# Optimization experiments

Measured on AMD Instinct MI355X. Metric: run time of the kernel, lower is better.

Reference implementation:

```python
import jax, jax.numpy as jnp
import numpy as np
from jax import lax

Q = 12           # sliding window size
IN_LEN = 336     # input_length
OUT_LEN = 336    # output_length


def setup_inputs() -> dict:
    key = jax.random.key(0)
    history_data = jax.random.normal(key, (64, IN_LEN, 862, 3), dtype=jnp.float32)
    return {"history_data": history_data}


def reference(history_data):
    # Maintain a rolling window of the last Q frames instead of torch.cat growth.
    window = history_data[:, -Q:, :, :]  # [B, Q, N, C]

    def step(w, _):
        m = jnp.mean(w, axis=1)  # [B, N, C]
        w = jnp.concatenate([w[:, 1:], m[:, None]], axis=1)  # shift window
        return w, m

    _, means = lax.scan(step, window, None, length=OUT_LEN)  # [O, B, N, C]
    prediction = jnp.transpose(means, (1, 0, 2, 3))  # [B, O, N, C]
    return prediction
```

## Files before the change

kernel.cpp:

```cpp
#include <hip/hip_runtime.h>


#define Q 12
#define IN_LEN 336
#define OUT_LEN 336
#define NB 64
#define SC (862 * 3)

__global__ __launch_bounds__(256) void
SimpleMovingAverage_22144851378808_kernel(const float* __restrict__ in,
                                          float* __restrict__ out) {
    const int tid = blockIdx.x * blockDim.x + threadIdx.x;
    if (tid >= NB * SC) return;
    const int b  = tid / SC;
    const int sc = tid - b * SC;

    const float* inp = in + ((size_t)(b * IN_LEN + (IN_LEN - Q)) * SC + sc);
    float w[Q];
#pragma unroll
    for (int k = 0; k < Q; ++k) w[k] = inp[(size_t)k * SC];

    float sum = 0.f;
#pragma unroll
    for (int k = 0; k < Q; ++k) sum += w[k];

    float* op = out + ((size_t)b * OUT_LEN * SC + sc);
    const float inv = 1.0f / (float)Q;

    for (int t = 0; t < OUT_LEN; t += Q) {
#pragma unroll
        for (int j = 0; j < Q; ++j) {
            const float m = sum * inv;
            sum += m - w[j];
            w[j] = m;
            op[(size_t)(t + j) * SC] = m;
        }
        float s = 0.f;
#pragma unroll
        for (int k = 0; k < Q; ++k) s += w[k];
        sum = s;
    }
}

extern "C" void kernel_launch(void* const* d_in, const int* in_sizes, int n_in,
                              void* d_out, int out_size, void* d_ws, size_t ws_size,
                              hipStream_t stream) {
    const float* in = (const float*)d_in[0];
    float* out = (float*)d_out;
    const int n_series = NB * SC;
    const int block = 256;
    const int grid = (n_series + block - 1) / block;
    SimpleMovingAverage_22144851378808_kernel<<<grid, block, 0, stream>>>(in, out);
}
```

Measured before the change: 346.0 us.

## Precompute linear SMA coefficients and apply them in parallel over output time

Because the recurrence is linear in the last Q inputs, a tiny kernel first computes a coefficient matrix of size OUT_LEN×Q by running the recurrence on unit vectors, storing it in the workspace. A second kernel then gives each thread a chunk of TT output steps and computes every output as a 12-term dot product with the loaded window. This removes the serial 336-step dependency per thread and adds parallelism across time chunks. The cost is that each block reloads the 12 input frames and the coefficients, adds a second launch, and changes the floating-point summation order.

```diff
diff --git a/kernel.cpp b/kernel.cpp
--- a/kernel.cpp
+++ b/kernel.cpp
@@ -6,25 +6,17 @@
 #define OUT_LEN 336
 #define NB 64
 #define SC (862 * 3)
+#define TT 12
 
-__global__ __launch_bounds__(256) void
-SimpleMovingAverage_22144851378808_kernel(const float* __restrict__ in,
-                                          float* __restrict__ out) {
-    const int tid = blockIdx.x * blockDim.x + threadIdx.x;
-    if (tid >= NB * SC) return;
-    const int b  = tid / SC;
-    const int sc = tid - b * SC;
+__global__ __launch_bounds__(64) void
+sma_coef_kernel(float* __restrict__ coef ) {
+    const int k = threadIdx.x;
+    if (k >= Q) return;
 
-    const float* inp = in + ((size_t)(b * IN_LEN + (IN_LEN - Q)) * SC + sc);
     float w[Q];
 #pragma unroll
-    for (int k = 0; k < Q; ++k) w[k] = inp[(size_t)k * SC];
-
-    float sum = 0.f;
-#pragma unroll
-    for (int k = 0; k < Q; ++k) sum += w[k];
-
-    float* op = out + ((size_t)b * OUT_LEN * SC + sc);
+    for (int j = 0; j < Q; ++j) w[j] = (j == k) ? 1.0f : 0.0f;
+    float sum = 1.0f;
     const float inv = 1.0f / (float)Q;
 
     for (int t = 0; t < OUT_LEN; t += Q) {
@@ -33,12 +25,37 @@
             const float m = sum * inv;
             sum += m - w[j];
             w[j] = m;
-            op[(size_t)(t + j) * SC] = m;
+            coef[(t + j) * Q + k] = m;
         }
         float s = 0.f;
 #pragma unroll
-        for (int k = 0; k < Q; ++k) s += w[k];
+        for (int j = 0; j < Q; ++j) s += w[j];
         sum = s;
+    }
+}
+
+__global__ __launch_bounds__(256) void
+sma_apply_kernel(const float* __restrict__ in,
+                 const float* __restrict__ coef,
+                 float* __restrict__ out) {
+    const int sc = blockIdx.x * blockDim.x + threadIdx.x;
+    if (sc >= SC) return;
+    const int b  = blockIdx.z;
+    const int t0 = blockIdx.y * TT;
+
+    const float* inp = in + ((size_t)(b * IN_LEN + (IN_LEN - Q)) * SC + sc);
+    float x[Q];
+#pragma unroll
+    for (int k = 0; k < Q; ++k) x[k] = inp[(size_t)k * SC];
+
+    float* op = out + ((size_t)(b * OUT_LEN + t0) * SC + sc);
+#pragma unroll
+    for (int j = 0; j < TT; ++j) {
+        const float* c = coef + (size_t)(t0 + j) * Q;
+        float acc = 0.f;
+#pragma unroll
+        for (int k = 0; k < Q; ++k) acc = fmaf(c[k], x[k], acc);
+        op[(size_t)j * SC] = acc;
     }
 }
 
@@ -46,9 +63,14 @@
                               void* d_out, int out_size, void* d_ws, size_t ws_size,
                               hipStream_t stream) {
     const float* in = (const float*)d_in[0];
-    float* out = (float*)d_out;
-    const int n_series = NB * SC;
+    float* out  = (float*)d_out;
+    float* coef = (float*)d_ws;
+
+    sma_coef_kernel<<<1, 64, 0, stream>>>(coef);
+
     const int block = 256;
-    const int grid = (n_series + block - 1) / block;
-    SimpleMovingAverage_22144851378808_kernel<<<grid, block, 0, stream>>>(in, out);
+    dim3 grid((SC + block - 1) / block,
+              OUT_LEN / TT,
+              NB);
+    sma_apply_kernel<<<grid, block, 0, stream>>>(in, coef, out);
 }
```

New measurement: 362.1 us. 1.05x slower.

## Replace sequential recurrence with precomputed linear coefficients and parallelize over time

Applied to the files above, without the earlier changes.

Each output step is a fixed linear combination of the last Q input frames, so the coefficients are now precomputed at compile time into a constant table. Every output is computed independently as a 12-term dot product, which lets the grid add a time dimension (OUT_LEN/TT blocks) and removes the serial dependency chain. Each thread also handles two adjacent channels through float2 loads and stores. The cost is that every time-block reloads the 12 input frames, and the arithmetic per output rises from a few ops to 24 FMAs. Rounding can differ slightly from the original recurrence.

```diff
diff --git a/kernel.cpp b/kernel.cpp
--- a/kernel.cpp
+++ b/kernel.cpp
@@ -5,50 +5,70 @@
 #define IN_LEN 336
 #define OUT_LEN 336
 #define NB 64
-#define SC (862 * 3)
+#define SC2 1293
+#define TT 12
+
+struct Coefs { float c[OUT_LEN][Q]; };
+
+constexpr Coefs make_coefs() {
+    Coefs tbl{};
+    for (int k = 0; k < Q; ++k) {
+        float w[Q] = {};
+        w[k] = 1.0f;
+        float sum = 1.0f;
+        for (int step = 0; step < OUT_LEN; ++step) {
+            const int j = step % Q;
+            const float m = sum * (1.0f / 12.0f);
+            sum += m - w[j];
+            w[j] = m;
+            tbl.c[step][k] = m;
+            if (j == Q - 1) {
+                float s = 0.0f;
+                for (int i = 0; i < Q; ++i) s += w[i];
+                sum = s;
+            }
+        }
+    }
+    return tbl;
+}
+
+__constant__ Coefs g_coef = make_coefs();
 
 __global__ __launch_bounds__(256) void
-SimpleMovingAverage_22144851378808_kernel(const float* __restrict__ in,
-                                          float* __restrict__ out) {
-    const int tid = blockIdx.x * blockDim.x + threadIdx.x;
-    if (tid >= NB * SC) return;
-    const int b  = tid / SC;
-    const int sc = tid - b * SC;
+SimpleMovingAverage_22144851378808_kernel(const float2* __restrict__ in,
+                                          float2* __restrict__ out) {
+    const int g = blockIdx.x * 256 + threadIdx.x;
+    if (g >= NB * SC2) return;
+    const int b  = g / SC2;
+    const int sc = g - b * SC2;
+    const int t0 = blockIdx.y * TT;
 
-    const float* inp = in + ((size_t)(b * IN_LEN + (IN_LEN - Q)) * SC + sc);
-    float w[Q];
+    const float2* ip = in + ((size_t)(b * IN_LEN + (IN_LEN - Q)) * SC2 + sc);
+    float2 x[Q];
 #pragma unroll
-    for (int k = 0; k < Q; ++k) w[k] = inp[(size_t)k * SC];
+    for (int k = 0; k < Q; ++k) x[k] = ip[(size_t)k * SC2];
 
-    float sum = 0.f;
+    float2* op = out + ((size_t)(b * OUT_LEN + t0) * SC2 + sc);
 #pragma unroll
-    for (int k = 0; k < Q; ++k) sum += w[k];
-
-    float* op = out + ((size_t)b * OUT_LEN * SC + sc);
-    const float inv = 1.0f / (float)Q;
-
-    for (int t = 0; t < OUT_LEN; t += Q) {
+    for (int j = 0; j < TT; ++j) {
+        float ax = 0.0f, ay = 0.0f;
 #pragma unroll
-        for (int j = 0; j < Q; ++j) {
-            const float m = sum * inv;
-            sum += m - w[j];
-            w[j] = m;
-            op[(size_t)(t + j) * SC] = m;
+        for (int k = 0; k < Q; ++k) {
+            const float ck = g_coef.c[t0 + j][k];
+            ax = fmaf(ck, x[k].x, ax);
+            ay = fmaf(ck, x[k].y, ay);
         }
-        float s = 0.f;
-#pragma unroll
-        for (int k = 0; k < Q; ++k) s += w[k];
-        sum = s;
+        op[(size_t)j * SC2] = make_float2(ax, ay);
     }
 }
 
 extern "C" void kernel_launch(void* const* d_in, const int* in_sizes, int n_in,
                               void* d_out, int out_size, void* d_ws, size_t ws_size,
                               hipStream_t stream) {
-    const float* in = (const float*)d_in[0];
-    float* out = (float*)d_out;
-    const int n_series = NB * SC;
-    const int block = 256;
-    const int grid = (n_series + block - 1) / block;
-    SimpleMovingAverage_22144851378808_kernel<<<grid, block, 0, stream>>>(in, out);
+    const float2* in = (const float2*)d_in[0];
+    float2* out = (float2*)d_out;
+    dim3 grid((NB * SC2 + 255) / 256,
+              OUT_LEN / TT,
+              1);
+    SimpleMovingAverage_22144851378808_kernel<<<grid, 256, 0, stream>>>(in, out);
 }
```

Measured after the change: 341.0 us. About the same (-1.4%).
